# Kernel tuning notes

Measured on AMD Instinct MI355X. Metric: run time of the kernel, lower is better.

Reference implementation:

```python
import jax, jax.numpy as jnp
import numpy as np

FEATURE_LEN = 64
DIM_ATOM = 256
DIM_GRAPH = 256
NUM_NEI = 32
B = 2048          # reactions / graphs in batch
ATOMS = 30        # atoms per molecule graph
N = B * ATOMS     # total nodes
E = 4 * N         # total edges
NMOL = 100000     # knowledge-graph molecule table size
S = 2             # molecules per reaction side (len(id_list))


def setup_inputs() -> dict:
    key = jax.random.key(0)
    ks = jax.random.split(key, 16)
    xavier = lambda k, shape: (jax.random.normal(k, shape, jnp.float32)
                               * np.sqrt(2.0 / (shape[0] + shape[-1])))
    return {
        "node_feat": jax.random.randint(ks[0], (N, 4), 0, FEATURE_LEN, jnp.int32),
        "edge_src": jax.random.randint(ks[1], (E,), 0, N, jnp.int32),
        "edge_dst": jax.random.randint(ks[2], (E,), 0, N, jnp.int32),
        "graph_ids": jnp.repeat(jnp.arange(B, dtype=jnp.int32), ATOMS),
        "id_list": jax.random.randint(ks[3], (S, B), 0, NMOL, jnp.int32),
        "id_list_target": jax.random.randint(ks[4], (S, B), 0, NMOL, jnp.int32),
        "all_mfea": (jax.random.uniform(ks[5], (NMOL, 40)) < 0.3).astype(jnp.float32),
        "neighbor_matrix": jax.random.randint(ks[6], (NMOL, NUM_NEI), 0, NMOL, jnp.int32),
        "W0": xavier(ks[7], (FEATURE_LEN, DIM_ATOM)),
        "b0": jnp.zeros((DIM_ATOM,), jnp.float32),
        "W1": xavier(ks[8], (DIM_ATOM, DIM_ATOM)),
        "b1": jnp.zeros((DIM_ATOM,), jnp.float32),
        "fea_emb": xavier(ks[9], (40, DIM_GRAPH)),
        "att_w": xavier(ks[10], (DIM_GRAPH, 1)),
        "att_b": jnp.zeros((1,), jnp.float32),
        "crosscl_w": xavier(ks[11], (DIM_GRAPH, DIM_ATOM)),
        "crosscl_b": jnp.zeros((DIM_ATOM,), jnp.float32),
    }


def reference(node_feat, edge_src, edge_dst, graph_ids, id_list, id_list_target,
              all_mfea, neighbor_matrix,
              W0, b0, W1, b1, fea_emb, att_w, att_b, crosscl_w, crosscl_b):
    n = node_feat.shape[0]
    # --- atom-level GCN (DGL GraphConv, norm='both') ---
    h = jax.nn.one_hot(node_feat, FEATURE_LEN, dtype=jnp.float32).sum(axis=1)  # [N, F]
    ones_e = jnp.ones((edge_src.shape[0],), jnp.float32)
    deg_out = jnp.clip(jax.ops.segment_sum(ones_e, edge_src, n), 1.0)
    deg_in = jnp.clip(jax.ops.segment_sum(ones_e, edge_dst, n), 1.0)
    norm_src = deg_out[:, None] ** -0.5
    norm_dst = deg_in[:, None] ** -0.5

    def gcn(x, W, b, act):
        m = (x * norm_src)[edge_src]                        # gather along edges
        agg = jax.ops.segment_sum(m, edge_dst, n)           # scatter-add
        z = (agg * norm_dst) @ W + b
        return act(z)

    h = gcn(h, W0, b0, jax.nn.relu)
    h = gcn(h, W1, b1, lambda z: z)
    # factor computed via python float() in torch -> detached constant
    factor = np.sqrt(DIM_ATOM).astype(np.float32) / jax.lax.stop_gradient(
        jnp.mean(jnp.linalg.norm(h, axis=1)))
    h = h * factor
    mol_atom_embedding = jax.ops.segment_sum(h, graph_ids, B)  # SumPooling [B, D]

    # --- reaction-level KG aggregation ---
    src_emb = jnp.einsum('sbf,fg->sbg', all_mfea[id_list], fea_emb)         # [S,B,G]
    tgt_emb = jnp.einsum('sbf,fg->sbg', all_mfea[id_list_target], fea_emb)  # [S,B,G]
    source_re = src_emb.mean(axis=0)   # 1/len * sum
    target_re = tgt_emb.mean(axis=0)

    item_emb = src_emb                                       # [S,B,G]
    nei_idx = neighbor_matrix[id_list]                       # [S,B,K]
    nei_emb = jnp.einsum('sbkf,fg->sbkg', all_mfea[nei_idx], fea_emb)  # [S,B,K,G]

    target_embedding = source_re + target_re                 # [B,G]
    score_nei = item_emb[:, :, None, :] * nei_emb * target_embedding[None, :, None, :]
    logits = score_nei @ att_w + att_b                       # [S,B,K,1]
    score_att = jax.nn.softmax(logits, axis=2)
    nei_agg = jnp.sum(score_att * nei_emb, axis=2)           # [S,B,G]

    mol_reaction_embedding = (item_emb + nei_agg).mean(axis=0)  # [B,G]
    mol_x_embedding = mol_reaction_embedding @ crosscl_w + crosscl_b
    mol_embedding = jnp.concatenate([mol_atom_embedding, mol_reaction_embedding], axis=1)
    return mol_embedding, mol_atom_embedding, mol_x_embedding
```

## Files before the change

kernel.cpp:

```cpp
#include <hip/hip_runtime.h>
#include <math.h>

#define N_NODES 61440
#define N_EDGES 245760
#define BATCH   2048
#define ATOMS   30
#define F_LEN   64
#define DIM     256
#define NUM_NEI 32
#define MF      40
#define ECAP    512
#define CH      32

typedef __attribute__((ext_vector_type(8))) short s8v;
typedef __attribute__((ext_vector_type(4))) float f4v;
typedef __attribute__((address_space(3))) unsigned lds_u32;
typedef const __attribute__((address_space(1))) unsigned glb_u32;

__device__ __forceinline__ unsigned short f2bf(float x) {
    union { float f; unsigned u; } c; c.f = x;
    unsigned r = (c.u + 0x7FFFu + ((c.u >> 16) & 1u)) >> 16;
    return (unsigned short)r;
}
__device__ __forceinline__ float bf2f(unsigned short u) {
    union { unsigned u; float f; } c; c.u = ((unsigned)u) << 16;
    return c.f;
}

__global__ void k_deg(const int* __restrict__ esrc, const int* __restrict__ edst,
                      int* deg_out, int* deg_in) {
    int e = blockIdx.x * 256 + threadIdx.x;
    if (e < N_EDGES) {
        atomicAdd(&deg_out[esrc[e]], 1);
        atomicAdd(&deg_in[edst[e]], 1);
    }
}

__global__ void k_alloc(const int* __restrict__ deg_in, int* row_start, int* cursor,
                        int* counter) {
    int t = threadIdx.x;
    int n = blockIdx.x * 256 + t;
    int lane = t & 63;
    int d = deg_in[n];
    int p = d;
#pragma unroll
    for (int o = 1; o < 64; o <<= 1) { int v = __shfl_up(p, o, 64); if (lane >= o) p += v; }
    int base = 0;
    if (lane == 63) base = atomicAdd(counter, p);
    base = __shfl(base, 63, 64);
    int v = base + p - d;
    row_start[n] = v;
    cursor[n] = v;
}

__global__ void k_csr_fill(const int* __restrict__ esrc, const int* __restrict__ edst,
                           int* cursor, int* csr_src) {
    int e = blockIdx.x * 256 + threadIdx.x;
    if (e < N_EDGES) {
        int p = atomicAdd(&cursor[edst[e]], 1);
        csr_src[p] = esrc[e];
    }
}

__global__ __launch_bounds__(256) void k_prepw(
    const float* __restrict__ W0, const float* __restrict__ W1,
    unsigned short* __restrict__ w0bt, unsigned short* __restrict__ w1bt) {
    __shared__ float tile[64][65];
    int bi = blockIdx.x;
    int t = threadIdx.x;
    int c = t & 63, rq = t >> 6;
    if (bi < 16) {
        int tr = bi >> 2, tc = bi & 3;
#pragma unroll 4
        for (int pass = 0; pass < 16; pass++) {
            int r = rq + 4 * pass;
            tile[r][c] = W1[(size_t)(tr * 64 + r) * 256 + tc * 64 + c];
        }
        __syncthreads();
#pragma unroll 4
        for (int pass = 0; pass < 16; pass++) {
            int nr = rq + 4 * pass;
            w1bt[(size_t)(tc * 64 + nr) * 256 + tr * 64 + c] = f2bf(tile[c][nr]);
        }
    } else {
        int tb = bi - 16;
#pragma unroll 4
        for (int pass = 0; pass < 16; pass++) {
            int r = rq + 4 * pass;
            tile[r][c] = W0[(size_t)r * 256 + tb * 64 + c];
        }
        __syncthreads();
#pragma unroll 4
        for (int pass = 0; pass < 16; pass++) {
            int nr = rq + 4 * pass;
            w0bt[(size_t)(tb * 64 + nr) * 64 + c] = f2bf(tile[c][nr]);
        }
    }
}

__global__ __launch_bounds__(256) void k_gcn0(
    const int* __restrict__ nf, const int* __restrict__ row_start,
    const int* __restrict__ csr_src, const int* __restrict__ deg_in,
    const int* __restrict__ deg_out, const unsigned short* __restrict__ w0bt,
    const float* __restrict__ b0, unsigned short* __restrict__ h1b) {
    __shared__ float la0[32 * 68];
    __shared__ int4  enf[ECAP];
    __shared__ float ens[ECAP];
    __shared__ int   rs[33];
    __shared__ float lnd[32], lns[32];
    __shared__ float b0c[256];
    int n0 = blockIdx.x * 32;
    int t = threadIdx.x;
    if (t < 32) rs[t] = row_start[n0 + t];
    if (t == 0) rs[32] = row_start[n0 + 31] + deg_in[n0 + 31];
    if (t < 32) {
        lnd[t] = rsqrtf((float)max(deg_in[n0 + t], 1));
        lns[t] = rsqrtf((float)max(deg_out[n0 + t], 1));
    }
    b0c[t] = b0[t];
    __syncthreads();
    int beg0 = rs[0];
    int tot = rs[32] - beg0; if (tot > ECAP) tot = ECAP;
    for (int e = t; e < tot; e += 256) {
        int s = csr_src[beg0 + e];
        enf[e] = ((const int4*)nf)[s];
        ens[e] = rsqrtf((float)max(deg_out[s], 1));
    }
    __syncthreads();
    {
        int row = t >> 3, kc = (t & 7) * 8;
        float a[8];
#pragma unroll
        for (int j = 0; j < 8; j++) a[j] = 0.f;
        int lo = rs[row] - beg0, hi = rs[row + 1] - beg0;
        if (hi > tot) hi = tot;
        for (int e = lo; e < hi; e++) {
            int4 f = enf[e]; float w = ens[e];
#pragma unroll
            for (int j = 0; j < 8; j++) {
                int k = kc + j;
                a[j] += w * (float)((f.x == k) + (f.y == k) + (f.z == k) + (f.w == k));
            }
        }
#pragma unroll
        for (int j = 0; j < 8; j++) la0[row * 68 + kc + j] = a[j];
    }
    __syncthreads();
    int lane = t & 63, wv = t >> 6;
    int ln = lane & 15, lg = lane >> 4;
    f4v acc[2][4];
#pragma unroll
    for (int mi = 0; mi < 2; mi++)
#pragma unroll
        for (int ni = 0; ni < 4; ni++) acc[mi][ni] = (f4v)0.f;
#pragma unroll
    for (int kst = 0; kst < 2; kst++) {
        s8v afr[2];
#pragma unroll
        for (int mi = 0; mi < 2; mi++) {
            const float* p = &la0[(mi * 16 + ln) * 68 + kst * 32 + lg * 8];
            f4v lo = *(const f4v*)p;
            f4v hi = *(const f4v*)(p + 4);
            s8v a;
#pragma unroll
            for (int j = 0; j < 4; j++) { a[j] = (short)f2bf(lo[j]); a[4 + j] = (short)f2bf(hi[j]); }
            afr[mi] = a;
        }
#pragma unroll
        for (int ni = 0; ni < 4; ni++) {
            int n = wv * 64 + ni * 16 + ln;
            s8v b = *(const s8v*)&w0bt[(size_t)n * 64 + kst * 32 + lg * 8];
            acc[0][ni] = __builtin_amdgcn_mfma_f32_16x16x32_bf16(afr[0], b, acc[0][ni], 0, 0, 0);
            acc[1][ni] = __builtin_amdgcn_mfma_f32_16x16x32_bf16(afr[1], b, acc[1][ni], 0, 0, 0);
        }
    }
#pragma unroll
    for (int mi = 0; mi < 2; mi++)
#pragma unroll
        for (int ni = 0; ni < 4; ni++) {
            int n = wv * 64 + ni * 16 + ln;
            float bb = b0c[n];
#pragma unroll
            for (int r = 0; r < 4; r++) {
                int m = mi * 16 + lg * 4 + r;
                float z = acc[mi][ni][r] * lnd[m] + bb;
                z = fmaxf(z, 0.f) * lns[m];
                h1b[(size_t)(n0 + m) * 256 + n] = f2bf(z);
            }
        }
}

__global__ __launch_bounds__(256, 4) void k_gcn1(
    const unsigned short* __restrict__ h1b, const int* __restrict__ row_start,
    const int* __restrict__ csr_src, const int* __restrict__ deg_in,
    const unsigned short* __restrict__ w1bt, const float* __restrict__ b1,
    unsigned short* __restrict__ h2b, float* __restrict__ partial) {
    __shared__ unsigned short stage[2 * CH * 256];
    __shared__ int   ecache[ECAP];
    __shared__ int   rs[33];
    __shared__ float lnd[32];
    __shared__ float b1c[256];
    __shared__ float nsq[32];
    unsigned short* lab = stage;
    int n0 = blockIdx.x * 32;
    int t = threadIdx.x;
    int lane = t & 63, wv = t >> 6;
    if (t < 32) rs[t] = row_start[n0 + t];
    if (t == 0) rs[32] = row_start[n0 + 31] + deg_in[n0 + 31];
    if (t < 32) {
        lnd[t] = rsqrtf((float)max(deg_in[n0 + t], 1));
        nsq[t] = 0.f;
    }
    b1c[t] = b1[t];
    __syncthreads();
    int beg0 = rs[0];
    int tot = rs[32] - beg0; if (tot > ECAP) tot = ECAP;
    for (int e = t; e < tot; e += 256) ecache[e] = csr_src[beg0 + e];
    __syncthreads();

    int gr = t >> 5;
    int gc = (t & 31) * 8;
    int lo[4], hi[4];
#pragma unroll
    for (int r = 0; r < 4; r++) {
        int i = gr + r * 8;
        lo[r] = rs[i] - beg0;
        int h = rs[i + 1] - beg0; if (h > tot) h = tot;
        hi[r] = h;
    }
    float a[4][8];
#pragma unroll
    for (int r = 0; r < 4; r++)
#pragma unroll
        for (int j = 0; j < 8; j++) a[r][j] = 0.f;

    int lhalf = lane >> 5;
    int colo = (lane & 31) * 8;
    int nc = (tot + CH - 1) >> 5;
#define ISSUE(c)                                                                   \
    {                                                                              \
        int base_ = (c) << 5;                                                      \
        unsigned short* sb_ = stage + ((c) & 1) * (CH * 256);                      \
        _Pragma("unroll")                                                          \
        for (int pp = 0; pp < 4; ++pp) {                                           \
            int p_ = wv + pp * 4;                                                  \
            int e_ = base_ + 2 * p_ + lhalf;                                       \
            int sv_ = ecache[min(e_, tot - 1)];                                    \
            __builtin_amdgcn_global_load_lds(                                      \
                (glb_u32*)(h1b + (size_t)sv_ * 256 + colo),                        \
                (lds_u32*)(sb_ + 2 * p_ * 256), 16, 0, 0);                         \
        }                                                                          \
    }
    if (nc > 0) ISSUE(0);
    for (int c = 0; c < nc; ++c) {
        if (c + 1 < nc) {
            ISSUE(c + 1);
            asm volatile("s_waitcnt vmcnt(4)" ::: "memory");
        } else {
            asm volatile("s_waitcnt vmcnt(0)" ::: "memory");
        }
        __builtin_amdgcn_sched_barrier(0);
        __builtin_amdgcn_s_barrier();
        int c0 = c << 5;
        int nch = min(CH, tot - c0);
        const unsigned short* sb = stage + (c & 1) * (CH * 256);
#pragma unroll
        for (int r = 0; r < 4; r++) {
            int es = max(lo[r] - c0, 0);
            int ee = min(hi[r] - c0, nch);
            for (int e = es; e < ee; e++) {
                s8v v = *(const s8v*)&sb[e * 256 + gc];
#pragma unroll
                for (int j = 0; j < 8; j++) a[r][j] += bf2f((unsigned short)v[j]);
            }
        }
        __builtin_amdgcn_s_barrier();
    }
#undef ISSUE
#pragma unroll
    for (int r = 0; r < 4; r++) {
        int i = gr + r * 8;
        s8v ov;
#pragma unroll
        for (int j = 0; j < 8; j++) ov[j] = (short)f2bf(a[r][j]);
        *(s8v*)&lab[i * 264 + gc] = ov;
    }
    __syncthreads();
    int ln = lane & 15, lg = lane >> 4;
    f4v acc[2][4];
#pragma unroll
    for (int mi = 0; mi < 2; mi++)
#pragma unroll
        for (int ni = 0; ni < 4; ni++) acc[mi][ni] = (f4v)0.f;
#pragma unroll 2
    for (int kst = 0; kst < 8; kst++) {
        s8v afr[2];
#pragma unroll
        for (int mi = 0; mi < 2; mi++)
            afr[mi] = *(const s8v*)&lab[(mi * 16 + ln) * 264 + kst * 32 + lg * 8];
#pragma unroll
        for (int ni = 0; ni < 4; ni++) {
            int n = wv * 64 + ni * 16 + ln;
            s8v b = *(const s8v*)&w1bt[(size_t)n * 256 + kst * 32 + lg * 8];
            acc[0][ni] = __builtin_amdgcn_mfma_f32_16x16x32_bf16(afr[0], b, acc[0][ni], 0, 0, 0);
            acc[1][ni] = __builtin_amdgcn_mfma_f32_16x16x32_bf16(afr[1], b, acc[1][ni], 0, 0, 0);
        }
    }
    float sm[2][4];
#pragma unroll
    for (int mi = 0; mi < 2; mi++)
#pragma unroll
        for (int r = 0; r < 4; r++) sm[mi][r] = 0.f;
#pragma unroll
    for (int mi = 0; mi < 2; mi++)
#pragma unroll
        for (int ni = 0; ni < 4; ni++) {
            int n = wv * 64 + ni * 16 + ln;
            float bb = b1c[n];
#pragma unroll
            for (int r = 0; r < 4; r++) {
                int m = mi * 16 + lg * 4 + r;
                float z = acc[mi][ni][r] * lnd[m] + bb;
                h2b[(size_t)(n0 + m) * 256 + n] = f2bf(z);
                sm[mi][r] += z * z;
            }
        }
#pragma unroll
    for (int mi = 0; mi < 2; mi++)
#pragma unroll
        for (int r = 0; r < 4; r++) {
            float v = sm[mi][r];
            v += __shfl_xor(v, 1);
            v += __shfl_xor(v, 2);
            v += __shfl_xor(v, 4);
            v += __shfl_xor(v, 8);
            if (ln == 0) atomicAdd(&nsq[mi * 16 + lg * 4 + r], v);
        }
    __syncthreads();
    if (t < 32) atomicAdd(&partial[(n0 + t) & 1023], sqrtf(nsq[t]));
}

__global__ void k_normfin(const float* __restrict__ partial, float* factor) {
    __shared__ float red[256];
    int t = threadIdx.x;
    float s = partial[t] + partial[t + 256] + partial[t + 512] + partial[t + 768];
    red[t] = s;
    __syncthreads();
    for (int o = 128; o; o >>= 1) {
        if (t < o) red[t] += red[t + o];
        __syncthreads();
    }
    if (t == 0) factor[0] = 16.0f / (red[0] / (float)N_NODES);
}

__global__ __launch_bounds__(256) void k_rxn(
    const int* __restrict__ id_list, const int* __restrict__ id_list_t,
    const int* __restrict__ neimat, const float* __restrict__ mfea,
    const float* __restrict__ fea_emb, const float* __restrict__ att_w,
    const float* __restrict__ att_b, const float* __restrict__ crosscl_w,
    const float* __restrict__ crosscl_b, const unsigned short* __restrict__ h2b,
    const float* __restrict__ factor, float* __restrict__ out) {
    __shared__ float com[MF];
    __shared__ float mitem[MF];
    __shared__ float u[DIM];
    __shared__ float nm[NUM_NEI * MF];
    __shared__ float vv[MF];
    __shared__ float aw[NUM_NEI];
    __shared__ float mre[DIM];
    int b = blockIdx.x;
    int t = threadIdx.x;
    int wv = t >> 6, lane = t & 63;
    float pv = 0.f;
    for (int a = 0; a < ATOMS; a++) pv += bf2f(h2b[(size_t)(b * ATOMS + a) * DIM + t]);
    pv *= factor[0];
    out[(size_t)b * 512 + t] = pv;
    out[(size_t)BATCH * 512 + (size_t)b * DIM + t] = pv;
    if (t < MF) {
        int i0 = id_list[b], i1 = id_list[BATCH + b];
        int j0 = id_list_t[b], j1 = id_list_t[BATCH + b];
        com[t] = 0.5f * (mfea[(size_t)i0 * MF + t] + mfea[(size_t)i1 * MF + t])
               + 0.5f * (mfea[(size_t)j0 * MF + t] + mfea[(size_t)j1 * MF + t]);
    }
    __syncthreads();
    float tg = 0.f;
    for (int f = 0; f < MF; f++) tg += com[f] * fea_emb[f * DIM + t];
    float awt = att_w[t];
    float msum = 0.f;
    for (int s = 0; s < 2; s++) {
        int id = id_list[s * BATCH + b];
        __syncthreads();
        if (t < MF) mitem[t] = mfea[(size_t)id * MF + t];
        for (int i = t; i < NUM_NEI * 10; i += 256) {
            int k = i / 10, q = i - k * 10;
            int nid = neimat[(size_t)id * NUM_NEI + k];
            *(float4*)&nm[k * MF + q * 4] = *(const float4*)&mfea[(size_t)nid * MF + q * 4];
        }
        __syncthreads();
        float item = 0.f;
        for (int f = 0; f < MF; f++) item += mitem[f] * fea_emb[f * DIM + t];
        u[t] = item * tg * awt;
        __syncthreads();
        for (int i = 0; i < 5; i++) {
            int f = wv + 8 * i;
            float p = 0.f;
#pragma unroll
            for (int j = 0; j < 4; j++) p += u[lane + 64 * j] * fea_emb[f * DIM + lane + 64 * j];
#pragma unroll
            for (int off = 32; off; off >>= 1) p += __shfl_down(p, off, 64);
            if (lane == 0) vv[f] = p;
        }
        __syncthreads();
        if (wv == 0) {
            float lg = -1e30f;
            if (lane < NUM_NEI) {
                lg = att_b[0];
                for (int f = 0; f < MF; f++) lg += nm[lane * MF + f] * vv[f];
            }
            float m = lg;
#pragma unroll
            for (int off = 16; off; off >>= 1) m = fmaxf(m, __shfl_xor(m, off, 32));
            float e = (lane < NUM_NEI) ? __expf(lg - m) : 0.f;
            float ssum = e;
#pragma unroll
            for (int off = 16; off; off >>= 1) ssum += __shfl_xor(ssum, off, 32);
            if (lane < NUM_NEI) aw[lane] = e / ssum;
        }
        __syncthreads();
        if (t < MF) {
            float w = 0.f;
            for (int k = 0; k < NUM_NEI; k++) w += aw[k] * nm[k * MF + t];
            vv[t] = w;
        }
        __syncthreads();
        float na = 0.f;
        for (int f = 0; f < MF; f++) na += vv[f] * fea_emb[f * DIM + t];
        msum += item + na;
    }
    float m = 0.5f * msum;
    out[(size_t)b * 512 + DIM + t] = m;
    mre[t] = m;
    __syncthreads();
    float acc = crosscl_b[t];
    for (int uu = 0; uu < DIM; uu++) acc += mre[uu] * crosscl_w[uu * DIM + t];
    out[(size_t)BATCH * 768 + (size_t)b * DIM + t] = acc;
}

extern "C" void kernel_launch(void* const* d_in, const int* in_sizes, int n_in,
                              void* d_out, int out_size, void* d_ws, size_t ws_size,
                              hipStream_t stream) {
    const int*   node_feat = (const int*)d_in[0];
    const int*   edge_src  = (const int*)d_in[1];
    const int*   edge_dst  = (const int*)d_in[2];
    const int*   id_list   = (const int*)d_in[4];
    const int*   id_list_t = (const int*)d_in[5];
    const float* all_mfea  = (const float*)d_in[6];
    const int*   neimat    = (const int*)d_in[7];
    const float* W0        = (const float*)d_in[8];
    const float* b0        = (const float*)d_in[9];
    const float* W1        = (const float*)d_in[10];
    const float* b1        = (const float*)d_in[11];
    const float* fea_emb   = (const float*)d_in[12];
    const float* att_w     = (const float*)d_in[13];
    const float* att_b     = (const float*)d_in[14];
    const float* crosscl_w = (const float*)d_in[15];
    const float* crosscl_b = (const float*)d_in[16];
    float* out = (float*)d_out;

    char* ws = (char*)d_ws;
    char* zbase = ws;
    int*   deg_out   = (int*)ws;            ws += (size_t)N_NODES * 4;
    int*   deg_in    = (int*)ws;            ws += (size_t)N_NODES * 4;
    float* partial   = (float*)ws;          ws += 1024 * 4;
    float* factor    = (float*)ws;
    int*   counter   = (int*)(ws + 8);      ws += 256;
    size_t zbytes = (size_t)(ws - zbase);
    int*   row_start = (int*)ws;            ws += (size_t)N_NODES * 4;
    int*   cursor    = (int*)ws;            ws += (size_t)N_NODES * 4;
    int*   csr_srcb  = (int*)ws;            ws += (size_t)N_EDGES * 4;
    unsigned short* w0bt = (unsigned short*)ws; ws += (size_t)256 * 64 * 2;
    unsigned short* w1bt = (unsigned short*)ws; ws += (size_t)256 * 256 * 2;
    unsigned short* h1b  = (unsigned short*)ws; ws += (size_t)N_NODES * DIM * 2;
    unsigned short* h2b  = (unsigned short*)ws; ws += (size_t)N_NODES * DIM * 2;

    hipMemsetAsync(zbase, 0, zbytes, stream);

    k_deg<<<(N_EDGES + 255) / 256, 256, 0, stream>>>(edge_src, edge_dst, deg_out, deg_in);
    k_alloc<<<N_NODES / 256, 256, 0, stream>>>(deg_in, row_start, cursor, counter);
    k_csr_fill<<<(N_EDGES + 255) / 256, 256, 0, stream>>>(edge_src, edge_dst, cursor, csr_srcb);
    k_prepw<<<20, 256, 0, stream>>>(W0, W1, w0bt, w1bt);

    k_gcn0<<<N_NODES / 32, 256, 0, stream>>>(node_feat, row_start, csr_srcb, deg_in,
                                             deg_out, w0bt, b0, h1b);
    k_gcn1<<<N_NODES / 32, 256, 0, stream>>>(h1b, row_start, csr_srcb, deg_in,
                                             w1bt, b1, h2b, partial);
    k_normfin<<<1, 256, 0, stream>>>(partial, factor);
    k_rxn<<<BATCH, 256, 0, stream>>>(id_list, id_list_t, neimat, all_mfea, fea_emb,
                                     att_w, att_b, crosscl_w, crosscl_b, h2b,
                                     factor, out);
}
```

Measured before the change: 179.6 us.

## Per-wave gather pipelines in GCN layer 1, split cross-CL GEMM out of rxn kernel

k_gcn1 now gives each wave its own 8 destination rows and its own double-buffered LDS staging region, with 16-edge chunks. This removes the block-wide s_barriers inside the aggregation loop, and each lane accumulates 4 columns using cheap bit-shift bf16 unpacking. k_rxn caches fea_emb in LDS and no longer performs the per-block 256x256 crosscl GEMV. That product moves to a new k_xgemm kernel that batches 8 rows per block to reuse weight loads. The cost is more LDS per block with lower occupancy (launch bounds 2), an extra kernel launch, and an extra workspace round trip for the reaction embeddings.

New measurement: 210.2 us. 17.0% more time.

```diff
diff --git a/kernel.cpp b/kernel.cpp
--- a/kernel.cpp
+++ b/kernel.cpp
@@ -10,7 +10,7 @@
 #define NUM_NEI 32
 #define MF      40
 #define ECAP    512
-#define CH      32
+#define CH      16
 
 typedef __attribute__((ext_vector_type(8))) short s8v;
 typedef __attribute__((ext_vector_type(4))) float f4v;
@@ -24,6 +24,10 @@
 }
 __device__ __forceinline__ float bf2f(unsigned short u) {
     union { unsigned u; float f; } c; c.u = ((unsigned)u) << 16;
+    return c.f;
+}
+__device__ __forceinline__ float u2f(unsigned u) {
+    union { unsigned u; float f; } c; c.u = u;
     return c.f;
 }
 
@@ -190,12 +194,12 @@
         }
 }
 
-__global__ __launch_bounds__(256, 4) void k_gcn1(
+__global__ __launch_bounds__(256, 2) void k_gcn1(
     const unsigned short* __restrict__ h1b, const int* __restrict__ row_start,
     const int* __restrict__ csr_src, const int* __restrict__ deg_in,
     const unsigned short* __restrict__ w1bt, const float* __restrict__ b1,
     unsigned short* __restrict__ h2b, float* __restrict__ partial) {
-    __shared__ unsigned short stage[2 * CH * 256];
+    __shared__ unsigned short stage[4 * 2 * CH * 256];
     __shared__ int   ecache[ECAP];
     __shared__ int   rs[33];
     __shared__ float lnd[32];
@@ -218,72 +222,72 @@
     for (int e = t; e < tot; e += 256) ecache[e] = csr_src[beg0 + e];
     __syncthreads();
 
-    int gr = t >> 5;
-    int gc = (t & 31) * 8;
-    int lo[4], hi[4];
-#pragma unroll
-    for (int r = 0; r < 4; r++) {
-        int i = gr + r * 8;
-        lo[r] = rs[i] - beg0;
-        int h = rs[i + 1] - beg0; if (h > tot) h = tot;
-        hi[r] = h;
-    }
-    float a[4][8];
-#pragma unroll
-    for (int r = 0; r < 4; r++)
-#pragma unroll
-        for (int j = 0; j < 8; j++) a[r][j] = 0.f;
-
+    int lo[8], hi[8];
+#pragma unroll
+    for (int r = 0; r < 8; r++) {
+        int l = rs[8 * wv + r] - beg0;     if (l > tot) l = tot;
+        int h = rs[8 * wv + r + 1] - beg0; if (h > tot) h = tot;
+        lo[r] = l; hi[r] = h;
+    }
+    int wlo = lo[0], whi = hi[7];
+    int nc = (whi - wlo + CH - 1) >> 4;
+    float a[8][4];
+#pragma unroll
+    for (int r = 0; r < 8; r++)
+#pragma unroll
+        for (int j = 0; j < 4; j++) a[r][j] = 0.f;
     int lhalf = lane >> 5;
     int colo = (lane & 31) * 8;
-    int nc = (tot + CH - 1) >> 5;
+    unsigned short* wstage = stage + wv * (2 * CH * 256);
+
 #define ISSUE(c)                                                                   \
     {                                                                              \
-        int base_ = (c) << 5;                                                      \
-        unsigned short* sb_ = stage + ((c) & 1) * (CH * 256);                      \
+        int base_ = wlo + (c) * CH;                                                \
+        unsigned short* sb_ = wstage + ((c) & 1) * (CH * 256);                     \
         _Pragma("unroll")                                                          \
-        for (int pp = 0; pp < 4; ++pp) {                                           \
-            int p_ = wv + pp * 4;                                                  \
-            int e_ = base_ + 2 * p_ + lhalf;                                       \
-            int sv_ = ecache[min(e_, tot - 1)];                                    \
+        for (int pp = 0; pp < 8; ++pp) {                                           \
+            int e_ = base_ + 2 * pp + lhalf;                                       \
+            int sv_ = ecache[min(e_, whi - 1)];                                    \
             __builtin_amdgcn_global_load_lds(                                      \
                 (glb_u32*)(h1b + (size_t)sv_ * 256 + colo),                        \
-                (lds_u32*)(sb_ + 2 * p_ * 256), 16, 0, 0);                         \
+                (lds_u32*)(sb_ + 2 * pp * 256), 16, 0, 0);                         \
         }                                                                          \
     }
     if (nc > 0) ISSUE(0);
     for (int c = 0; c < nc; ++c) {
         if (c + 1 < nc) {
             ISSUE(c + 1);
-            asm volatile("s_waitcnt vmcnt(4)" ::: "memory");
+            asm volatile("s_waitcnt vmcnt(8)" ::: "memory");
         } else {
             asm volatile("s_waitcnt vmcnt(0)" ::: "memory");
         }
         __builtin_amdgcn_sched_barrier(0);
-        __builtin_amdgcn_s_barrier();
-        int c0 = c << 5;
-        int nch = min(CH, tot - c0);
-        const unsigned short* sb = stage + (c & 1) * (CH * 256);
-#pragma unroll
-        for (int r = 0; r < 4; r++) {
-            int es = max(lo[r] - c0, 0);
-            int ee = min(hi[r] - c0, nch);
+        int c0g = wlo + c * CH;
+        int nch = min(CH, whi - c0g);
+        const unsigned short* sb = wstage + (c & 1) * (CH * 256);
+#pragma unroll
+        for (int r = 0; r < 8; r++) {
+            int es = max(lo[r] - c0g, 0);
+            int ee = min(hi[r] - c0g, nch);
             for (int e = es; e < ee; e++) {
-                s8v v = *(const s8v*)&sb[e * 256 + gc];
-#pragma unroll
-                for (int j = 0; j < 8; j++) a[r][j] += bf2f((unsigned short)v[j]);
+                const unsigned* p = (const unsigned*)(sb + e * 256 + lane * 4);
+                unsigned p0 = p[0], p1 = p[1];
+                a[r][0] += u2f(p0 << 16);
+                a[r][1] += u2f(p0 & 0xffff0000u);
+                a[r][2] += u2f(p1 << 16);
+                a[r][3] += u2f(p1 & 0xffff0000u);
             }
         }
-        __builtin_amdgcn_s_barrier();
     }
 #undef ISSUE
-#pragma unroll
-    for (int r = 0; r < 4; r++) {
-        int i = gr + r * 8;
-        s8v ov;
-#pragma unroll
-        for (int j = 0; j < 8; j++) ov[j] = (short)f2bf(a[r][j]);
-        *(s8v*)&lab[i * 264 + gc] = ov;
+    __syncthreads();
+#pragma unroll
+    for (int r = 0; r < 8; r++) {
+        int i = 8 * wv + r;
+        unsigned lo2 = (unsigned)f2bf(a[r][0]) | ((unsigned)f2bf(a[r][1]) << 16);
+        unsigned hi2 = (unsigned)f2bf(a[r][2]) | ((unsigned)f2bf(a[r][3]) << 16);
+        unsigned* dst = (unsigned*)&lab[(size_t)i * 264 + lane * 4];
+        dst[0] = lo2; dst[1] = hi2;
     }
     __syncthreads();
     int ln = lane & 15, lg = lane >> 4;
@@ -357,19 +361,21 @@
     const int* __restrict__ id_list, const int* __restrict__ id_list_t,
     const int* __restrict__ neimat, const float* __restrict__ mfea,
     const float* __restrict__ fea_emb, const float* __restrict__ att_w,
-    const float* __restrict__ att_b, const float* __restrict__ crosscl_w,
-    const float* __restrict__ crosscl_b, const unsigned short* __restrict__ h2b,
-    const float* __restrict__ factor, float* __restrict__ out) {
+    const float* __restrict__ att_b, const unsigned short* __restrict__ h2b,
+    const float* __restrict__ factor, float* __restrict__ mre_out,
+    float* __restrict__ out) {
+    __shared__ float femb[MF * DIM];
     __shared__ float com[MF];
     __shared__ float mitem[MF];
     __shared__ float u[DIM];
     __shared__ float nm[NUM_NEI * MF];
     __shared__ float vv[MF];
     __shared__ float aw[NUM_NEI];
-    __shared__ float mre[DIM];
     int b = blockIdx.x;
     int t = threadIdx.x;
     int wv = t >> 6, lane = t & 63;
+    for (int i = t; i < MF * DIM / 4; i += 256)
+        ((float4*)femb)[i] = ((const float4*)fea_emb)[i];
     float pv = 0.f;
     for (int a = 0; a < ATOMS; a++) pv += bf2f(h2b[(size_t)(b * ATOMS + a) * DIM + t]);
     pv *= factor[0];
@@ -383,7 +389,7 @@
     }
     __syncthreads();
     float tg = 0.f;
-    for (int f = 0; f < MF; f++) tg += com[f] * fea_emb[f * DIM + t];
+    for (int f = 0; f < MF; f++) tg += com[f] * femb[f * DIM + t];
     float awt = att_w[t];
     float msum = 0.f;
     for (int s = 0; s < 2; s++) {
@@ -397,14 +403,14 @@
         }
         __syncthreads();
         float item = 0.f;
-        for (int f = 0; f < MF; f++) item += mitem[f] * fea_emb[f * DIM + t];
+        for (int f = 0; f < MF; f++) item += mitem[f] * femb[f * DIM + t];
         u[t] = item * tg * awt;
         __syncthreads();
         for (int i = 0; i < 5; i++) {
             int f = wv + 8 * i;
             float p = 0.f;
 #pragma unroll
-            for (int j = 0; j < 4; j++) p += u[lane + 64 * j] * fea_emb[f * DIM + lane + 64 * j];
+            for (int j = 0; j < 4; j++) p += u[lane + 64 * j] * femb[f * DIM + lane + 64 * j];
 #pragma unroll
             for (int off = 32; off; off >>= 1) p += __shfl_down(p, off, 64);
             if (lane == 0) vv[f] = p;
@@ -433,16 +439,35 @@
         }
         __syncthreads();
         float na = 0.f;
-        for (int f = 0; f < MF; f++) na += vv[f] * fea_emb[f * DIM + t];
+        for (int f = 0; f < MF; f++) na += vv[f] * femb[f * DIM + t];
         msum += item + na;
     }
     float m = 0.5f * msum;
     out[(size_t)b * 512 + DIM + t] = m;
-    mre[t] = m;
-    __syncthreads();
-    float acc = crosscl_b[t];
-    for (int uu = 0; uu < DIM; uu++) acc += mre[uu] * crosscl_w[uu * DIM + t];
-    out[(size_t)BATCH * 768 + (size_t)b * DIM + t] = acc;
+    mre_out[(size_t)b * DIM + t] = m;
+}
+
+__global__ __launch_bounds__(256) void k_xgemm(
+    const float* __restrict__ mre, const float* __restrict__ cw,
+    const float* __restrict__ cb, float* __restrict__ out) {
+    __shared__ float lm[8 * DIM];
+    int b0 = blockIdx.x * 8;
+    int t = threadIdx.x;
+    for (int i = t; i < 8 * DIM / 4; i += 256)
+        ((float4*)lm)[i] = ((const float4*)(mre + (size_t)b0 * DIM))[i];
+    __syncthreads();
+    float acc[8];
+    float bb = cb[t];
+#pragma unroll
+    for (int i = 0; i < 8; i++) acc[i] = bb;
+    for (int uu = 0; uu < DIM; uu++) {
+        float w = cw[(size_t)uu * DIM + t];
+#pragma unroll
+        for (int i = 0; i < 8; i++) acc[i] += lm[i * DIM + uu] * w;
+    }
+#pragma unroll
+    for (int i = 0; i < 8; i++)
+        out[(size_t)BATCH * 768 + (size_t)(b0 + i) * DIM + t] = acc[i];
 }
 
 extern "C" void kernel_launch(void* const* d_in, const int* in_sizes, int n_in,
@@ -481,6 +506,7 @@
     unsigned short* w1bt = (unsigned short*)ws; ws += (size_t)256 * 256 * 2;
     unsigned short* h1b  = (unsigned short*)ws; ws += (size_t)N_NODES * DIM * 2;
     unsigned short* h2b  = (unsigned short*)ws; ws += (size_t)N_NODES * DIM * 2;
+    float* mre       = (float*)ws;          ws += (size_t)BATCH * DIM * 4;
 
     hipMemsetAsync(zbase, 0, zbytes, stream);
 
@@ -495,6 +521,6 @@
                                              w1bt, b1, h2b, partial);
     k_normfin<<<1, 256, 0, stream>>>(partial, factor);
     k_rxn<<<BATCH, 256, 0, stream>>>(id_list, id_list_t, neimat, all_mfea, fea_emb,
-                                     att_w, att_b, crosscl_w, crosscl_b, h2b,
-                                     factor, out);
-}
+                                     att_w, att_b, h2b, factor, mre, out);
+    k_xgemm<<<BATCH / 8, 256, 0, stream>>>(mre, crosscl_w, crosscl_b, out);
+}
```

## Fuse GCN layer-1 with reaction KG aggregation and batch final projection

Applied to the files above, without the earlier changes.

Merges the degree-count and weight-prep kernels into one launch. Runs the independent reaction-level attention blocks alongside the second GCN layer by interleaving them in a single grid. The norm finalisation, graph pooling and cross-projection move into a new kernel that handles 8 graphs per block, so each crosscl_w load is reused across those 8 graphs. The first layer's one-hot aggregation now uses LDS atomics instead of 64-wide compare loops. This removes launch gaps and serialization, at the cost of an extra workspace buffer for mre, a mixed-role kernel that reserves the larger shared-memory footprint for every block, and LDS atomic contention.

New measurement: 198.2 us. 1.1x slower.

```diff
diff --git a/kernel.cpp b/kernel.cpp
--- a/kernel.cpp
+++ b/kernel.cpp
@@ -11,6 +11,7 @@
 #define MF      40
 #define ECAP    512
 #define CH      32
+#define NBG     (N_NODES / 32)
 
 typedef __attribute__((ext_vector_type(8))) short s8v;
 typedef __attribute__((ext_vector_type(4))) float f4v;
@@ -26,13 +27,53 @@
     union { unsigned u; float f; } c; c.u = ((unsigned)u) << 16;
     return c.f;
 }
-
-__global__ void k_deg(const int* __restrict__ esrc, const int* __restrict__ edst,
-                      int* deg_out, int* deg_in) {
-    int e = blockIdx.x * 256 + threadIdx.x;
-    if (e < N_EDGES) {
+__device__ __forceinline__ float u2f(unsigned u) {
+    union { unsigned u; float f; } c; c.u = u;
+    return c.f;
+}
+
+__global__ __launch_bounds__(256) void k_deg_prepw(
+    const int* __restrict__ esrc, const int* __restrict__ edst,
+    int* deg_out, int* deg_in,
+    const float* __restrict__ W0, const float* __restrict__ W1,
+    unsigned short* __restrict__ w0bt, unsigned short* __restrict__ w1bt) {
+    __shared__ float tile[64][65];
+    int bi = blockIdx.x;
+    int t = threadIdx.x;
+    if (bi < 960) {
+        int e = bi * 256 + t;
         atomicAdd(&deg_out[esrc[e]], 1);
         atomicAdd(&deg_in[edst[e]], 1);
+        return;
+    }
+    int b2 = bi - 960;
+    int c = t & 63, rq = t >> 6;
+    if (b2 < 16) {
+        int tr = b2 >> 2, tc = b2 & 3;
+#pragma unroll 4
+        for (int pass = 0; pass < 16; pass++) {
+            int r = rq + 4 * pass;
+            tile[r][c] = W1[(size_t)(tr * 64 + r) * 256 + tc * 64 + c];
+        }
+        __syncthreads();
+#pragma unroll 4
+        for (int pass = 0; pass < 16; pass++) {
+            int nr = rq + 4 * pass;
+            w1bt[(size_t)(tc * 64 + nr) * 256 + tr * 64 + c] = f2bf(tile[c][nr]);
+        }
+    } else {
+        int tb = b2 - 16;
+#pragma unroll 4
+        for (int pass = 0; pass < 16; pass++) {
+            int r = rq + 4 * pass;
+            tile[r][c] = W0[(size_t)r * 256 + tb * 64 + c];
+        }
+        __syncthreads();
+#pragma unroll 4
+        for (int pass = 0; pass < 16; pass++) {
+            int nr = rq + 4 * pass;
+            w0bt[(size_t)(tb * 64 + nr) * 64 + c] = f2bf(tile[c][nr]);
+        }
     }
 }
 
@@ -59,42 +100,6 @@
     if (e < N_EDGES) {
         int p = atomicAdd(&cursor[edst[e]], 1);
         csr_src[p] = esrc[e];
-    }
-}
-
-__global__ __launch_bounds__(256) void k_prepw(
-    const float* __restrict__ W0, const float* __restrict__ W1,
-    unsigned short* __restrict__ w0bt, unsigned short* __restrict__ w1bt) {
-    __shared__ float tile[64][65];
-    int bi = blockIdx.x;
-    int t = threadIdx.x;
-    int c = t & 63, rq = t >> 6;
-    if (bi < 16) {
-        int tr = bi >> 2, tc = bi & 3;
-#pragma unroll 4
-        for (int pass = 0; pass < 16; pass++) {
-            int r = rq + 4 * pass;
-            tile[r][c] = W1[(size_t)(tr * 64 + r) * 256 + tc * 64 + c];
-        }
-        __syncthreads();
-#pragma unroll 4
-        for (int pass = 0; pass < 16; pass++) {
-            int nr = rq + 4 * pass;
-            w1bt[(size_t)(tc * 64 + nr) * 256 + tr * 64 + c] = f2bf(tile[c][nr]);
-        }
-    } else {
-        int tb = bi - 16;
-#pragma unroll 4
-        for (int pass = 0; pass < 16; pass++) {
-            int r = rq + 4 * pass;
-            tile[r][c] = W0[(size_t)r * 256 + tb * 64 + c];
-        }
-        __syncthreads();
-#pragma unroll 4
-        for (int pass = 0; pass < 16; pass++) {
-            int nr = rq + 4 * pass;
-            w0bt[(size_t)(tb * 64 + nr) * 64 + c] = f2bf(tile[c][nr]);
-        }
     }
 }
 
@@ -118,6 +123,7 @@
         lns[t] = rsqrtf((float)max(deg_out[n0 + t], 1));
     }
     b0c[t] = b0[t];
+    for (int i = t; i < 32 * 68; i += 256) la0[i] = 0.f;
     __syncthreads();
     int beg0 = rs[0];
     int tot = rs[32] - beg0; if (tot > ECAP) tot = ECAP;
@@ -127,23 +133,15 @@
         ens[e] = rsqrtf((float)max(deg_out[s], 1));
     }
     __syncthreads();
-    {
-        int row = t >> 3, kc = (t & 7) * 8;
-        float a[8];
-#pragma unroll
-        for (int j = 0; j < 8; j++) a[j] = 0.f;
+    if (t < 128) {
+        int row = t >> 2, fi = t & 3;
         int lo = rs[row] - beg0, hi = rs[row + 1] - beg0;
         if (hi > tot) hi = tot;
         for (int e = lo; e < hi; e++) {
-            int4 f = enf[e]; float w = ens[e];
-#pragma unroll
-            for (int j = 0; j < 8; j++) {
-                int k = kc + j;
-                a[j] += w * (float)((f.x == k) + (f.y == k) + (f.z == k) + (f.w == k));
-            }
-        }
-#pragma unroll
-        for (int j = 0; j < 8; j++) la0[row * 68 + kc + j] = a[j];
+            int4 f = enf[e];
+            int fv = (fi == 0) ? f.x : (fi == 1) ? f.y : (fi == 2) ? f.z : f.w;
+            atomicAdd(&la0[row * 68 + fv], ens[e]);
+        }
     }
     __syncthreads();
     int lane = t & 63, wv = t >> 6;
@@ -190,159 +188,249 @@
         }
 }
 
-__global__ __launch_bounds__(256, 4) void k_gcn1(
+__global__ __launch_bounds__(256, 4) void k_gcn1rxn(
     const unsigned short* __restrict__ h1b, const int* __restrict__ row_start,
     const int* __restrict__ csr_src, const int* __restrict__ deg_in,
     const unsigned short* __restrict__ w1bt, const float* __restrict__ b1,
-    unsigned short* __restrict__ h2b, float* __restrict__ partial) {
-    __shared__ unsigned short stage[2 * CH * 256];
-    __shared__ int   ecache[ECAP];
-    __shared__ int   rs[33];
-    __shared__ float lnd[32];
-    __shared__ float b1c[256];
-    __shared__ float nsq[32];
-    unsigned short* lab = stage;
-    int n0 = blockIdx.x * 32;
+    unsigned short* __restrict__ h2b, float* __restrict__ partial,
+    const int* __restrict__ id_list, const int* __restrict__ id_list_t,
+    const int* __restrict__ neimat, const float* __restrict__ mfea,
+    const float* __restrict__ fea_emb, const float* __restrict__ att_w,
+    const float* __restrict__ att_b, float* __restrict__ mre_out,
+    float* __restrict__ out) {
+    __shared__ __attribute__((aligned(16))) char smem[36992];
+    int bid = blockIdx.x;
     int t = threadIdx.x;
     int lane = t & 63, wv = t >> 6;
-    if (t < 32) rs[t] = row_start[n0 + t];
-    if (t == 0) rs[32] = row_start[n0 + 31] + deg_in[n0 + 31];
-    if (t < 32) {
-        lnd[t] = rsqrtf((float)max(deg_in[n0 + t], 1));
-        nsq[t] = 0.f;
-    }
-    b1c[t] = b1[t];
-    __syncthreads();
-    int beg0 = rs[0];
-    int tot = rs[32] - beg0; if (tot > ECAP) tot = ECAP;
-    for (int e = t; e < tot; e += 256) ecache[e] = csr_src[beg0 + e];
-    __syncthreads();
-
-    int gr = t >> 5;
-    int gc = (t & 31) * 8;
-    int lo[4], hi[4];
-#pragma unroll
-    for (int r = 0; r < 4; r++) {
-        int i = gr + r * 8;
-        lo[r] = rs[i] - beg0;
-        int h = rs[i + 1] - beg0; if (h > tot) h = tot;
-        hi[r] = h;
-    }
-    float a[4][8];
-#pragma unroll
-    for (int r = 0; r < 4; r++)
-#pragma unroll
-        for (int j = 0; j < 8; j++) a[r][j] = 0.f;
-
-    int lhalf = lane >> 5;
-    int colo = (lane & 31) * 8;
-    int nc = (tot + CH - 1) >> 5;
+    bool isg; int sub;
+    if (bid < 2 * NBG) { isg = !(bid & 1); sub = bid >> 1; }
+    else { isg = false; sub = NBG + (bid - 2 * NBG); }
+
+    if (isg) {
+        unsigned short* stage = (unsigned short*)smem;
+        int*   ecache = (int*)(smem + 32768);
+        int*   rs     = (int*)(smem + 34816);
+        float* lnd    = (float*)(smem + 34960);
+        float* b1c    = (float*)(smem + 35088);
+        float* nsq    = (float*)(smem + 36112);
+        unsigned short* lab = stage;
+        int n0 = sub * 32;
+        if (t < 32) rs[t] = row_start[n0 + t];
+        if (t == 0) rs[32] = row_start[n0 + 31] + deg_in[n0 + 31];
+        if (t < 32) {
+            lnd[t] = rsqrtf((float)max(deg_in[n0 + t], 1));
+            nsq[t] = 0.f;
+        }
+        b1c[t] = b1[t];
+        __syncthreads();
+        int beg0 = rs[0];
+        int tot = rs[32] - beg0; if (tot > ECAP) tot = ECAP;
+        for (int e = t; e < tot; e += 256) ecache[e] = csr_src[beg0 + e];
+        __syncthreads();
+
+        int gr = t >> 5;
+        int gc = (t & 31) * 8;
+        int lo[4], hi[4];
+#pragma unroll
+        for (int r = 0; r < 4; r++) {
+            int i = gr + r * 8;
+            lo[r] = rs[i] - beg0;
+            int h = rs[i + 1] - beg0; if (h > tot) h = tot;
+            hi[r] = h;
+        }
+        float a[4][8];
+#pragma unroll
+        for (int r = 0; r < 4; r++)
+#pragma unroll
+            for (int j = 0; j < 8; j++) a[r][j] = 0.f;
+
+        int lhalf = lane >> 5;
+        int colo = (lane & 31) * 8;
+        int nc = (tot + CH - 1) >> 5;
 #define ISSUE(c)                                                                   \
-    {                                                                              \
-        int base_ = (c) << 5;                                                      \
-        unsigned short* sb_ = stage + ((c) & 1) * (CH * 256);                      \
-        _Pragma("unroll")                                                          \
-        for (int pp = 0; pp < 4; ++pp) {                                           \
-            int p_ = wv + pp * 4;                                                  \
-            int e_ = base_ + 2 * p_ + lhalf;                                       \
-            int sv_ = ecache[min(e_, tot - 1)];                                    \
-            __builtin_amdgcn_global_load_lds(                                      \
-                (glb_u32*)(h1b + (size_t)sv_ * 256 + colo),                        \
-                (lds_u32*)(sb_ + 2 * p_ * 256), 16, 0, 0);                         \
-        }                                                                          \
-    }
-    if (nc > 0) ISSUE(0);
-    for (int c = 0; c < nc; ++c) {
-        if (c + 1 < nc) {
-            ISSUE(c + 1);
-            asm volatile("s_waitcnt vmcnt(4)" ::: "memory");
-        } else {
-            asm volatile("s_waitcnt vmcnt(0)" ::: "memory");
-        }
-        __builtin_amdgcn_sched_barrier(0);
-        __builtin_amdgcn_s_barrier();
-        int c0 = c << 5;
-        int nch = min(CH, tot - c0);
-        const unsigned short* sb = stage + (c & 1) * (CH * 256);
+        {                                                                          \
+            int base_ = (c) << 5;                                                  \
+            unsigned short* sb_ = stage + ((c) & 1) * (CH * 256);                  \
+            _Pragma("unroll")                                                      \
+            for (int pp = 0; pp < 4; ++pp) {                                       \
+                int p_ = wv + pp * 4;                                              \
+                int e_ = base_ + 2 * p_ + lhalf;                                   \
+                int sv_ = ecache[min(e_, tot - 1)];                                \
+                __builtin_amdgcn_global_load_lds(                                  \
+                    (glb_u32*)(h1b + (size_t)sv_ * 256 + colo),                    \
+                    (lds_u32*)(sb_ + 2 * p_ * 256), 16, 0, 0);                     \
+            }                                                                      \
+        }
+        if (nc > 0) ISSUE(0);
+        for (int c = 0; c < nc; ++c) {
+            if (c + 1 < nc) {
+                ISSUE(c + 1);
+                asm volatile("s_waitcnt vmcnt(4)" ::: "memory");
+            } else {
+                asm volatile("s_waitcnt vmcnt(0)" ::: "memory");
+            }
+            __builtin_amdgcn_sched_barrier(0);
+            __builtin_amdgcn_s_barrier();
+            int c0 = c << 5;
+            int nch = min(CH, tot - c0);
+            const unsigned short* sb = stage + (c & 1) * (CH * 256);
+#pragma unroll
+            for (int r = 0; r < 4; r++) {
+                int es = max(lo[r] - c0, 0);
+                int ee = min(hi[r] - c0, nch);
+                for (int e = es; e < ee; e++) {
+                    s8v v = *(const s8v*)&sb[e * 256 + gc];
+#pragma unroll
+                    for (int j = 0; j < 8; j++) a[r][j] += bf2f((unsigned short)v[j]);
+                }
+            }
+            __builtin_amdgcn_s_barrier();
+        }
+#undef ISSUE
 #pragma unroll
         for (int r = 0; r < 4; r++) {
-            int es = max(lo[r] - c0, 0);
-            int ee = min(hi[r] - c0, nch);
-            for (int e = es; e < ee; e++) {
-                s8v v = *(const s8v*)&sb[e * 256 + gc];
-#pragma unroll
-                for (int j = 0; j < 8; j++) a[r][j] += bf2f((unsigned short)v[j]);
-            }
-        }
-        __builtin_amdgcn_s_barrier();
-    }
-#undef ISSUE
-#pragma unroll
-    for (int r = 0; r < 4; r++) {
-        int i = gr + r * 8;
-        s8v ov;
-#pragma unroll
-        for (int j = 0; j < 8; j++) ov[j] = (short)f2bf(a[r][j]);
-        *(s8v*)&lab[i * 264 + gc] = ov;
-    }
-    __syncthreads();
-    int ln = lane & 15, lg = lane >> 4;
-    f4v acc[2][4];
-#pragma unroll
-    for (int mi = 0; mi < 2; mi++)
-#pragma unroll
-        for (int ni = 0; ni < 4; ni++) acc[mi][ni] = (f4v)0.f;
+            int i = gr + r * 8;
+            s8v ov;
+#pragma unroll
+            for (int j = 0; j < 8; j++) ov[j] = (short)f2bf(a[r][j]);
+            *(s8v*)&lab[i * 264 + gc] = ov;
+        }
+        __syncthreads();
+        int ln = lane & 15, lg = lane >> 4;
+        f4v acc[2][4];
+#pragma unroll
+        for (int mi = 0; mi < 2; mi++)
+#pragma unroll
+            for (int ni = 0; ni < 4; ni++) acc[mi][ni] = (f4v)0.f;
 #pragma unroll 2
-    for (int kst = 0; kst < 8; kst++) {
-        s8v afr[2];
+        for (int kst = 0; kst < 8; kst++) {
+            s8v afr[2];
+#pragma unroll
+            for (int mi = 0; mi < 2; mi++)
+                afr[mi] = *(const s8v*)&lab[(mi * 16 + ln) * 264 + kst * 32 + lg * 8];
+#pragma unroll
+            for (int ni = 0; ni < 4; ni++) {
+                int n = wv * 64 + ni * 16 + ln;
+                s8v b = *(const s8v*)&w1bt[(size_t)n * 256 + kst * 32 + lg * 8];
+                acc[0][ni] = __builtin_amdgcn_mfma_f32_16x16x32_bf16(afr[0], b, acc[0][ni], 0, 0, 0);
+                acc[1][ni] = __builtin_amdgcn_mfma_f32_16x16x32_bf16(afr[1], b, acc[1][ni], 0, 0, 0);
+            }
+        }
+        float sm[2][4];
 #pragma unroll
         for (int mi = 0; mi < 2; mi++)
-            afr[mi] = *(const s8v*)&lab[(mi * 16 + ln) * 264 + kst * 32 + lg * 8];
-#pragma unroll
-        for (int ni = 0; ni < 4; ni++) {
-            int n = wv * 64 + ni * 16 + ln;
-            s8v b = *(const s8v*)&w1bt[(size_t)n * 256 + kst * 32 + lg * 8];
-            acc[0][ni] = __builtin_amdgcn_mfma_f32_16x16x32_bf16(afr[0], b, acc[0][ni], 0, 0, 0);
-            acc[1][ni] = __builtin_amdgcn_mfma_f32_16x16x32_bf16(afr[1], b, acc[1][ni], 0, 0, 0);
-        }
-    }
-    float sm[2][4];
-#pragma unroll
-    for (int mi = 0; mi < 2; mi++)
-#pragma unroll
-        for (int r = 0; r < 4; r++) sm[mi][r] = 0.f;
-#pragma unroll
-    for (int mi = 0; mi < 2; mi++)
-#pragma unroll
-        for (int ni = 0; ni < 4; ni++) {
-            int n = wv * 64 + ni * 16 + ln;
-            float bb = b1c[n];
+#pragma unroll
+            for (int r = 0; r < 4; r++) sm[mi][r] = 0.f;
+#pragma unroll
+        for (int mi = 0; mi < 2; mi++)
+#pragma unroll
+            for (int ni = 0; ni < 4; ni++) {
+                int n = wv * 64 + ni * 16 + ln;
+                float bb = b1c[n];
+#pragma unroll
+                for (int r = 0; r < 4; r++) {
+                    int m = mi * 16 + lg * 4 + r;
+                    float z = acc[mi][ni][r] * lnd[m] + bb;
+                    h2b[(size_t)(n0 + m) * 256 + n] = f2bf(z);
+                    sm[mi][r] += z * z;
+                }
+            }
+#pragma unroll
+        for (int mi = 0; mi < 2; mi++)
 #pragma unroll
             for (int r = 0; r < 4; r++) {
-                int m = mi * 16 + lg * 4 + r;
-                float z = acc[mi][ni][r] * lnd[m] + bb;
-                h2b[(size_t)(n0 + m) * 256 + n] = f2bf(z);
-                sm[mi][r] += z * z;
-            }
-        }
-#pragma unroll
-    for (int mi = 0; mi < 2; mi++)
-#pragma unroll
-        for (int r = 0; r < 4; r++) {
-            float v = sm[mi][r];
-            v += __shfl_xor(v, 1);
-            v += __shfl_xor(v, 2);
-            v += __shfl_xor(v, 4);
-            v += __shfl_xor(v, 8);
-            if (ln == 0) atomicAdd(&nsq[mi * 16 + lg * 4 + r], v);
-        }
-    __syncthreads();
-    if (t < 32) atomicAdd(&partial[(n0 + t) & 1023], sqrtf(nsq[t]));
-}
-
-__global__ void k_normfin(const float* __restrict__ partial, float* factor) {
+                float v = sm[mi][r];
+                v += __shfl_xor(v, 1);
+                v += __shfl_xor(v, 2);
+                v += __shfl_xor(v, 4);
+                v += __shfl_xor(v, 8);
+                if (ln == 0) atomicAdd(&nsq[mi * 16 + lg * 4 + r], v);
+            }
+        __syncthreads();
+        if (t < 32) atomicAdd(&partial[(n0 + t) & 1023], sqrtf(nsq[t]));
+    } else {
+        float* com   = (float*)smem;
+        float* mitem = (float*)(smem + 160);
+        float* u     = (float*)(smem + 320);
+        float* nm    = (float*)(smem + 1344);
+        float* vv    = (float*)(smem + 6464);
+        float* aw    = (float*)(smem + 6624);
+        int b = sub;
+        if (t < MF) {
+            int i0 = id_list[b], i1 = id_list[BATCH + b];
+            int j0 = id_list_t[b], j1 = id_list_t[BATCH + b];
+            com[t] = 0.5f * (mfea[(size_t)i0 * MF + t] + mfea[(size_t)i1 * MF + t])
+                   + 0.5f * (mfea[(size_t)j0 * MF + t] + mfea[(size_t)j1 * MF + t]);
+        }
+        __syncthreads();
+        float tg = 0.f;
+        for (int f = 0; f < MF; f++) tg += com[f] * fea_emb[f * DIM + t];
+        float awt = att_w[t];
+        float msum = 0.f;
+        for (int s = 0; s < 2; s++) {
+            int id = id_list[s * BATCH + b];
+            __syncthreads();
+            if (t < MF) mitem[t] = mfea[(size_t)id * MF + t];
+            for (int i = t; i < NUM_NEI * 10; i += 256) {
+                int k = i / 10, q = i - k * 10;
+                int nid = neimat[(size_t)id * NUM_NEI + k];
+                *(float4*)&nm[k * MF + q * 4] = *(const float4*)&mfea[(size_t)nid * MF + q * 4];
+            }
+            __syncthreads();
+            float item = 0.f;
+            for (int f = 0; f < MF; f++) item += mitem[f] * fea_emb[f * DIM + t];
+            u[t] = item * tg * awt;
+            __syncthreads();
+            for (int i = 0; i < 5; i++) {
+                int f = wv + 8 * i;
+                float p = 0.f;
+#pragma unroll
+                for (int j = 0; j < 4; j++) p += u[lane + 64 * j] * fea_emb[f * DIM + lane + 64 * j];
+#pragma unroll
+                for (int off = 32; off; off >>= 1) p += __shfl_down(p, off, 64);
+                if (lane == 0) vv[f] = p;
+            }
+            __syncthreads();
+            if (wv == 0) {
+                float lg2 = -1e30f;
+                if (lane < NUM_NEI) {
+                    lg2 = att_b[0];
+                    for (int f = 0; f < MF; f++) lg2 += nm[lane * MF + f] * vv[f];
+                }
+                float m = lg2;
+#pragma unroll
+                for (int off = 16; off; off >>= 1) m = fmaxf(m, __shfl_xor(m, off, 32));
+                float e = (lane < NUM_NEI) ? __expf(lg2 - m) : 0.f;
+                float ssum = e;
+#pragma unroll
+                for (int off = 16; off; off >>= 1) ssum += __shfl_xor(ssum, off, 32);
+                if (lane < NUM_NEI) aw[lane] = e / ssum;
+            }
+            __syncthreads();
+            if (t < MF) {
+                float w = 0.f;
+                for (int k = 0; k < NUM_NEI; k++) w += aw[k] * nm[k * MF + t];
+                vv[t] = w;
+            }
+            __syncthreads();
+            float na = 0.f;
+            for (int f = 0; f < MF; f++) na += vv[f] * fea_emb[f * DIM + t];
+            msum += item + na;
+        }
+        float m = 0.5f * msum;
+        out[(size_t)b * 512 + DIM + t] = m;
+        mre_out[(size_t)b * DIM + t] = m;
+    }
+}
+
+__global__ __launch_bounds__(256) void k_fin(
+    const unsigned short* __restrict__ h2b, const float* __restrict__ partial,
+    const float* __restrict__ mre, const float* __restrict__ cw,
+    const float* __restrict__ cb, float* __restrict__ out) {
     __shared__ float red[256];
+    __shared__ float lm[8 * DIM];
     int t = threadIdx.x;
+    int b0 = blockIdx.x * 8;
     float s = partial[t] + partial[t + 256] + partial[t + 512] + partial[t + 768];
     red[t] = s;
     __syncthreads();
@@ -350,99 +438,31 @@
         if (t < o) red[t] += red[t + o];
         __syncthreads();
     }
-    if (t == 0) factor[0] = 16.0f / (red[0] / (float)N_NODES);
-}
-
-__global__ __launch_bounds__(256) void k_rxn(
-    const int* __restrict__ id_list, const int* __restrict__ id_list_t,
-    const int* __restrict__ neimat, const float* __restrict__ mfea,
-    const float* __restrict__ fea_emb, const float* __restrict__ att_w,
-    const float* __restrict__ att_b, const float* __restrict__ crosscl_w,
-    const float* __restrict__ crosscl_b, const unsigned short* __restrict__ h2b,
-    const float* __restrict__ factor, float* __restrict__ out) {
-    __shared__ float com[MF];
-    __shared__ float mitem[MF];
-    __shared__ float u[DIM];
-    __shared__ float nm[NUM_NEI * MF];
-    __shared__ float vv[MF];
-    __shared__ float aw[NUM_NEI];
-    __shared__ float mre[DIM];
-    int b = blockIdx.x;
-    int t = threadIdx.x;
-    int wv = t >> 6, lane = t & 63;
-    float pv = 0.f;
-    for (int a = 0; a < ATOMS; a++) pv += bf2f(h2b[(size_t)(b * ATOMS + a) * DIM + t]);
-    pv *= factor[0];
-    out[(size_t)b * 512 + t] = pv;
-    out[(size_t)BATCH * 512 + (size_t)b * DIM + t] = pv;
-    if (t < MF) {
-        int i0 = id_list[b], i1 = id_list[BATCH + b];
-        int j0 = id_list_t[b], j1 = id_list_t[BATCH + b];
-        com[t] = 0.5f * (mfea[(size_t)i0 * MF + t] + mfea[(size_t)i1 * MF + t])
-               + 0.5f * (mfea[(size_t)j0 * MF + t] + mfea[(size_t)j1 * MF + t]);
-    }
+    float fac = 16.0f * (float)N_NODES / red[0];
+#pragma unroll 2
+    for (int i = 0; i < 8; i++) {
+        float pv = 0.f;
+        for (int a = 0; a < ATOMS; a++)
+            pv += bf2f(h2b[(size_t)((b0 + i) * ATOMS + a) * DIM + t]);
+        pv *= fac;
+        out[(size_t)(b0 + i) * 512 + t] = pv;
+        out[(size_t)BATCH * 512 + (size_t)(b0 + i) * DIM + t] = pv;
+    }
+    for (int i = t; i < 8 * DIM / 4; i += 256)
+        ((float4*)lm)[i] = ((const float4*)(mre + (size_t)b0 * DIM))[i];
     __syncthreads();
-    float tg = 0.f;
-    for (int f = 0; f < MF; f++) tg += com[f] * fea_emb[f * DIM + t];
-    float awt = att_w[t];
-    float msum = 0.f;
-    for (int s = 0; s < 2; s++) {
-        int id = id_list[s * BATCH + b];
-        __syncthreads();
-        if (t < MF) mitem[t] = mfea[(size_t)id * MF + t];
-        for (int i = t; i < NUM_NEI * 10; i += 256) {
-            int k = i / 10, q = i - k * 10;
-            int nid = neimat[(size_t)id * NUM_NEI + k];
-            *(float4*)&nm[k * MF + q * 4] = *(const float4*)&mfea[(size_t)nid * MF + q * 4];
-        }
-        __syncthreads();
-        float item = 0.f;
-        for (int f = 0; f < MF; f++) item += mitem[f] * fea_emb[f * DIM + t];
-        u[t] = item * tg * awt;
-        __syncthreads();
-        for (int i = 0; i < 5; i++) {
-            int f = wv + 8 * i;
-            float p = 0.f;
-#pragma unroll
-            for (int j = 0; j < 4; j++) p += u[lane + 64 * j] * fea_emb[f * DIM + lane + 64 * j];
-#pragma unroll
-            for (int off = 32; off; off >>= 1) p += __shfl_down(p, off, 64);
-            if (lane == 0) vv[f] = p;
-        }
-        __syncthreads();
-        if (wv == 0) {
-            float lg = -1e30f;
-            if (lane < NUM_NEI) {
-                lg = att_b[0];
-                for (int f = 0; f < MF; f++) lg += nm[lane * MF + f] * vv[f];
-            }
-            float m = lg;
-#pragma unroll
-            for (int off = 16; off; off >>= 1) m = fmaxf(m, __shfl_xor(m, off, 32));
-            float e = (lane < NUM_NEI) ? __expf(lg - m) : 0.f;
-            float ssum = e;
-#pragma unroll
-            for (int off = 16; off; off >>= 1) ssum += __shfl_xor(ssum, off, 32);
-            if (lane < NUM_NEI) aw[lane] = e / ssum;
-        }
-        __syncthreads();
-        if (t < MF) {
-            float w = 0.f;
-            for (int k = 0; k < NUM_NEI; k++) w += aw[k] * nm[k * MF + t];
-            vv[t] = w;
-        }
-        __syncthreads();
-        float na = 0.f;
-        for (int f = 0; f < MF; f++) na += vv[f] * fea_emb[f * DIM + t];
-        msum += item + na;
-    }
-    float m = 0.5f * msum;
-    out[(size_t)b * 512 + DIM + t] = m;
-    mre[t] = m;
-    __syncthreads();
-    float acc = crosscl_b[t];
-    for (int uu = 0; uu < DIM; uu++) acc += mre[uu] * crosscl_w[uu * DIM + t];
-    out[(size_t)BATCH * 768 + (size_t)b * DIM + t] = acc;
+    float acc[8];
+    float bb = cb[t];
+#pragma unroll
+    for (int i = 0; i < 8; i++) acc[i] = bb;
+    for (int uu = 0; uu < DIM; uu++) {
+        float w = cw[(size_t)uu * DIM + t];
+#pragma unroll
+        for (int i = 0; i < 8; i++) acc[i] += lm[i * DIM + uu] * w;
+    }
+#pragma unroll
+    for (int i = 0; i < 8; i++)
+        out[(size_t)BATCH * 768 + (size_t)(b0 + i) * DIM + t] = acc[i];
 }
 
 extern "C" void kernel_launch(void* const* d_in, const int* in_sizes, int n_in,
@@ -471,7 +491,6 @@
     int*   deg_out   = (int*)ws;            ws += (size_t)N_NODES * 4;
     int*   deg_in    = (int*)ws;            ws += (size_t)N_NODES * 4;
     float* partial   = (float*)ws;          ws += 1024 * 4;
-    float* factor    = (float*)ws;
     int*   counter   = (int*)(ws + 8);      ws += 256;
     size_t zbytes = (size_t)(ws - zbase);
     int*   row_start = (int*)ws;            ws += (size_t)N_NODES * 4;
@@ -481,20 +500,18 @@
     unsigned short* w1bt = (unsigned short*)ws; ws += (size_t)256 * 256 * 2;
     unsigned short* h1b  = (unsigned short*)ws; ws += (size_t)N_NODES * DIM * 2;
     unsigned short* h2b  = (unsigned short*)ws; ws += (size_t)N_NODES * DIM * 2;
+    float* mre       = (float*)ws;          ws += (size_t)BATCH * DIM * 4;
 
     hipMemsetAsync(zbase, 0, zbytes, stream);
 
-    k_deg<<<(N_EDGES + 255) / 256, 256, 0, stream>>>(edge_src, edge_dst, deg_out, deg_in);
+    k_deg_prepw<<<980, 256, 0, stream>>>(edge_src, edge_dst, deg_out, deg_in,
+                                         W0, W1, w0bt, w1bt);
     k_alloc<<<N_NODES / 256, 256, 0, stream>>>(deg_in, row_start, cursor, counter);
     k_csr_fill<<<(N_EDGES + 255) / 256, 256, 0, stream>>>(edge_src, edge_dst, cursor, csr_srcb);
-    k_prepw<<<20, 256, 0, stream>>>(W0, W1, w0bt, w1bt);
-
     k_gcn0<<<N_NODES / 32, 256, 0, stream>>>(node_feat, row_start, csr_srcb, deg_in,
                                              deg_out, w0bt, b0, h1b);
-    k_gcn1<<<N_NODES / 32, 256, 0, stream>>>(h1b, row_start, csr_srcb, deg_in,
-                                             w1bt, b1, h2b, partial);
-    k_normfin<<<1, 256, 0, stream>>>(partial, factor);
-    k_rxn<<<BATCH, 256, 0, stream>>>(id_list, id_list_t, neimat, all_mfea, fea_emb,
-                                     att_w, att_b, crosscl_w, crosscl_b, h2b,
-                                     factor, out);
-}
+    k_gcn1rxn<<<2 * NBG + (BATCH - NBG), 256, 0, stream>>>(
+        h1b, row_start, csr_srcb, deg_in, w1bt, b1, h2b, partial,
+        id_list, id_list_t, neimat, all_mfea, fea_emb, att_w, att_b, mre, out);
+    k_fin<<<BATCH / 8, 256, 0, stream>>>(h2b, partial, mre, crosscl_w, crosscl_b, out);
+}
```
